# Kernel optimization log

Measured on AMD Instinct MI355X. Metric: run time of the kernel, lower is better.

## Reference

```python
import jax, jax.numpy as jnp
import numpy as np

B, N, T, NUM_API = 4, 160, 512, 20000  # queries, list length, tag vocab size, number of APIs
TAG_DENSITY = 0.05


def _compute_lambda(y_score, tag_set, M):
    # y_score: [N]; tag_set: [N,T] multi-hot rows api_tag_embedding[y_pred]; M: [T] multi-hot target.
    # Faithful to mode == 'cover' branch of LambdaRankLoss.compute_lambda.
    n = tag_set.shape[0]
    f32 = tag_set.dtype
    idx = jnp.arange(n)
    log_values = jnp.log2(jnp.arange(2, n + 2, dtype=f32))             # [N]
    P = jax.lax.cummax(tag_set, axis=0)                                # set_union_list = cummax(tag_set) [N,T]
    Mc = (jnp.count_nonzero(M) + 1).astype(f32)                        # M_nonzero_count
    # count_nonzero(clamp(M - set_union_list[k], min=0)) == #(M_t > P[k,t])
    cU = jnp.sum(M[None, :] > P, axis=1).astype(f32)                   # [N]

    # pre[i] = rowwise-max of tag_set[:i-1]. Torch quirk: i==0 -> tag_set[:-1] (all but last row); i==1 -> empty.
    pre = jnp.where(idx[:, None] == 0, P[n - 2][None, :],
                    jnp.where(idx[:, None] == 1, jnp.zeros((), f32),
                              P[jnp.clip(idx - 2, 0, n - 1)]))         # [N,T] (0 is max-identity: entries >= 0)

    # R[a,b] = max(tag_set[a..b]) along rows; 0 when b < a (rows before a masked to 0, then cummax)
    masked = jnp.where(idx[None, :, None] >= idx[:, None, None], tag_set[None, :, :], jnp.zeros((), f32))
    R = jax.lax.cummax(masked, axis=1)                                 # [N,N,T]

    # mid[k,i] = max(tag_set[i+1:k]) = R[i+1, k-1] when k >= i+2, else empty -> 0
    i_ix = idx[None, :]
    k_ix = idx[:, None]
    mid = jnp.where((k_ix >= i_ix + 2)[:, :, None],
                    R[jnp.clip(i_ix + 1, 0, n - 1), jnp.clip(k_ix - 1, 0, n - 1)],
                    jnp.zeros((), f32))                                # [K,I,T]

    # A[k,i] = max(cat(tag_set[:i-1], tag_set[i+1:k]));  Q[k,i,j] = max(A[k,i], tag_set[j])
    A = jnp.maximum(pre[None, :, :], mid)                              # [K,I,T]
    # count_nonzero(clamp(M - Q[k,i,j], 0)) = sum_t [M_t > A[k,i,t]] * [M_t > tag_set[j,t]]
    aM = (M[None, None, :] > A).astype(f32)                            # [K,I,T]
    bM = (M[None, :] > tag_set).astype(f32)                            # [J,T]
    cQ = jnp.einsum('kit,jt->kij', aM, bM)                             # [K,I,J] Q_nonzero counts

    W = (cU[:, None, None] - cQ) / (Mc * log_values[:, None, None])    # [K,I,J]
    # Z1[i,j] = sum_{k=i}^{j-1} W[k,i,j]  (strictly upper-triangular in (i,j))
    maskZ = (idx[None, :, None] <= idx[:, None, None]) & (idx[:, None, None] < idx[None, None, :])
    Z1 = jnp.sum(jnp.where(maskZ, W, jnp.zeros((), f32)), axis=0)      # [I,J]

    # lambda1[i,j] = 1 / (1 + exp(s_i - s_j))
    lam = 1.0 / (1.0 + jnp.exp(y_score[:, None] - y_score[None, :]))
    return jnp.sum(lam * Z1) / jnp.asarray(n + 1, f32)


def setup_inputs() -> dict:
    key = jax.random.key(0)
    k1, k2, k3, k4 = jax.random.split(key, 4)
    y_scores = jax.random.normal(k1, (B, N), jnp.float32)
    y_preds = jax.random.randint(k2, (B, N), 0, NUM_API)
    M = (jax.random.uniform(k3, (B, T)) < TAG_DENSITY).astype(jnp.float32)
    api_tag_embedding = (jax.random.uniform(k4, (NUM_API, T)) < TAG_DENSITY).astype(jnp.float32)
    return {"y_scores": y_scores, "M": M, "api_tag_embedding": api_tag_embedding, "y_preds": y_preds}


def reference(y_scores, M, api_tag_embedding, y_preds):
    def per_query(s, m, pred):
        return _compute_lambda(s, api_tag_embedding[pred], m)
    vals = jax.vmap(per_query)(y_scores, M, y_preds)  # [B]
    return jnp.mean(vals)  # loss / len(y_scores)
```

## Files before the change

### kernel.cpp

```cpp
#include <hip/hip_runtime.h>
#include <stdint.h>

typedef unsigned long long u64;

constexpr int B_ = 4;
constexpr int N_ = 160;
constexpr int T_ = 512;
constexpr int W_ = T_ / 64;

__global__ __launch_bounds__(64) void pack_tags(const float* __restrict__ emb,
                                                const int* __restrict__ preds,
                                                u64* __restrict__ tags) {
    int row  = blockIdx.x;
    int lane = threadIdx.x;
    const float* src = emb + (long long)preds[row] * T_;
#pragma unroll
    for (int w = 0; w < W_; ++w) {
        float v = src[w * 64 + lane];
        u64 m = __ballot(v != 0.0f);
        if (lane == 0) tags[(long long)row * W_ + w] = m;
    }
}

__global__ __launch_bounds__(256) void pack_scan(const float* __restrict__ Mf,
                                                 const u64* __restrict__ tags,
                                                 u64* __restrict__ Mp,
                                                 u64* __restrict__ P,
                                                 float* __restrict__ cU,
                                                 float* __restrict__ Mc) {
    __shared__ u64 S0[N_ * W_];
    __shared__ u64 S1[N_ * W_];
    __shared__ u64 Msh[W_];

    const int b    = blockIdx.x;
    const int tid  = threadIdx.x;
    const int lane = tid & 63;
    const int wv   = tid >> 6;

    for (int w = wv; w < W_; w += 4) {
        float v = Mf[(long long)b * T_ + w * 64 + lane];
        u64 m = __ballot(v != 0.0f);
        if (lane == 0) { Msh[w] = m; Mp[b * W_ + w] = m; }
    }
    for (int x = tid; x < N_ * W_; x += 256)
        S0[x] = tags[(long long)b * N_ * W_ + x];
    __syncthreads();

    u64* src = S0;
    u64* dst = S1;
    for (int d = 1; d < N_; d <<= 1) {
        for (int x = tid; x < N_ * W_; x += 256) {
            int r = x >> 3;
            u64 v = src[x];
            if (r >= d) v |= src[x - d * W_];
            dst[x] = v;
        }
        __syncthreads();
        u64* t = src; src = dst; dst = t;
    }

    for (int x = tid; x < N_ * W_; x += 256)
        P[(long long)b * N_ * W_ + x] = src[x];

    if (tid < N_) {
        int c = 0;
#pragma unroll
        for (int w = 0; w < W_; ++w)
            c += __popcll(Msh[w] & ~src[tid * W_ + w]);
        cU[b * N_ + tid] = (float)c;
    }
    if (tid == 0) {
        int c = 0;
#pragma unroll
        for (int w = 0; w < W_; ++w) c += __popcll(Msh[w]);
        Mc[b] = (float)(c + 1);
    }
}

__global__ __launch_bounds__(256) void lambda_main(const u64* __restrict__ tags,
                                                   const u64* __restrict__ Mp,
                                                   const u64* __restrict__ P,
                                                   const float* __restrict__ cU,
                                                   const float* __restrict__ Mc,
                                                   const float* __restrict__ scores,
                                                   double* __restrict__ partials) {
    constexpr int LD = N_ + 1;
    __shared__ u64 tagsT[W_ * LD];
    __shared__ u64 bufA[W_ * LD];
    __shared__ u64 bufB[W_ * LD];
    __shared__ u64 awT[W_ * LD];
    __shared__ u64 bT[W_ * LD];
    __shared__ u64 Msh[W_];
    __shared__ float scoresL[N_];
    __shared__ float redF[4];

    const int k   = blockIdx.x;
    const int b   = blockIdx.y;
    const int tid = threadIdx.x;

    if (tid < W_)  Msh[tid]    = Mp[b * W_ + tid];
    if (tid < N_)  scoresL[tid] = scores[b * N_ + tid];

    for (int x = tid; x < W_ * N_; x += 256) {
        int r = x >> 3, w = x & 7;
        tagsT[w * LD + r] = tags[(long long)b * N_ * W_ + x];
    }
    __syncthreads();

    for (int x = tid; x < W_ * N_; x += 256) {
        int r = x >> 3, w = x & 7;
        bufA[w * LD + r] = (r < k) ? tagsT[w * LD + r] : 0ull;
    }
    __syncthreads();

    u64* src = bufA;
    u64* dst = bufB;
    for (int d = 1; d < N_; d <<= 1) {
        for (int x = tid; x < W_ * N_; x += 256) {
            int r = x >> 3, w = x & 7;
            u64 v = src[w * LD + r];
            if (r + d < k) v |= src[w * LD + r + d];
            dst[w * LD + r] = v;
        }
        __syncthreads();
        u64* t = src; src = dst; dst = t;
    }

    for (int x = tid; x < W_ * N_; x += 256) {
        int i = x >> 3, w = x & 7;
        u64 pre;
        if (i == 1) pre = 0ull;
        else {
            int sr = (i == 0) ? (N_ - 2) : (i - 2);
            pre = P[((long long)b * N_ + sr) * W_ + w];
        }
        u64 sv = (i + 1 < k) ? src[w * LD + i + 1] : 0ull;
        awT[w * LD + i] = Msh[w] & ~pre & ~sv;
        bT[w * LD + i]  = Msh[w] & ~tagsT[w * LD + i];
    }
    __syncthreads();

    const int m = N_ - 1 - k;
    float accLam = 0.0f, accC = 0.0f;
    if (m > 0) {
        const int npairs = (k + 1) * m;
        if (tid < npairs) {
            int cnt = (npairs - tid + 255) >> 8;
            int i   = tid / m;
            int jj  = tid - i * m;
            const int di = 256 / m;
            const int rj = 256 - di * m;
            for (int c = 0; c < cnt; ++c) {
                const int j = k + 1 + jj;
                int cc = 0;
#pragma unroll
                for (int w = 0; w < W_; ++w)
                    cc += __popcll(awT[w * LD + i] & bT[w * LD + j]);
                float lam = 1.0f / (1.0f + __expf(scoresL[i] - scoresL[j]));
                accLam += lam;
                accC   += lam * (float)cc;
                i += di; jj += rj;
                if (jj >= m) { jj -= m; ++i; }
            }
        }
    }

    const float cUk = cU[b * N_ + k];
    float val = cUk * accLam - accC;
    for (int off = 32; off >= 1; off >>= 1) val += __shfl_down(val, off, 64);
    if ((tid & 63) == 0) redF[tid >> 6] = val;
    __syncthreads();
    if (tid == 0) {
        float s = redF[0] + redF[1] + redF[2] + redF[3];
        float invlog = 1.0f / log2f((float)(k + 2));
        partials[b * N_ + k] = (double)(s * invlog) / (double)Mc[b];
    }
}

__global__ __launch_bounds__(256) void finalize(const double* __restrict__ partials,
                                                float* __restrict__ out) {
    __shared__ double redD[4];
    const int tid = threadIdx.x;
    double s = 0.0;
    for (int x = tid; x < B_ * N_; x += 256) s += partials[x];
    for (int off = 32; off >= 1; off >>= 1) s += __shfl_down(s, off, 64);
    if ((tid & 63) == 0) redD[tid >> 6] = s;
    __syncthreads();
    if (tid == 0) {
        double t = redD[0] + redD[1] + redD[2] + redD[3];
        out[0] = (float)(t / ((double)(N_ + 1) * (double)B_));
    }
}

extern "C" void kernel_launch(void* const* d_in, const int* in_sizes, int n_in,
                              void* d_out, int out_size, void* d_ws, size_t ws_size,
                              hipStream_t stream) {
    const float* y_scores = (const float*)d_in[0];
    const float* Mf       = (const float*)d_in[1];
    const float* emb      = (const float*)d_in[2];
    const int*   preds    = (const int*)d_in[3];
    float* out = (float*)d_out;

    u64* tags = (u64*)d_ws;
    u64* P    = tags + (size_t)B_ * N_ * W_;
    u64* Mp   = P + (size_t)B_ * N_ * W_;
    double* partials = (double*)(Mp + B_ * W_);
    float* cU = (float*)(partials + B_ * N_);
    float* Mc = cU + B_ * N_;

    pack_tags<<<B_ * N_, 64, 0, stream>>>(emb, preds, tags);
    pack_scan<<<B_, 256, 0, stream>>>(Mf, tags, Mp, P, cU, Mc);
    dim3 grid(N_, B_);
    lambda_main<<<grid, 256, 0, stream>>>(tags, Mp, P, cU, Mc, y_scores, partials);
    finalize<<<1, 256, 0, stream>>>(partials, out);
}
```

Baseline: 113.6 us.

## Fuse pipeline into two kernels with in-block prefix scan and atomic final reduction

```diff
diff --git a/kernel.cpp b/kernel.cpp
--- a/kernel.cpp
+++ b/kernel.cpp
@@ -8,135 +8,118 @@
 constexpr int T_ = 512;
 constexpr int W_ = T_ / 64;
 
-__global__ __launch_bounds__(64) void pack_tags(const float* __restrict__ emb,
-                                                const int* __restrict__ preds,
-                                                u64* __restrict__ tags) {
+__global__ __launch_bounds__(64) void pack_all(const float* __restrict__ emb,
+                                               const int* __restrict__ preds,
+                                               const float* __restrict__ Mf,
+                                               u64* __restrict__ tags,
+                                               u64* __restrict__ Mp,
+                                               double* __restrict__ accD,
+                                               int* __restrict__ cnt) {
     int row  = blockIdx.x;
     int lane = threadIdx.x;
-    const float* src = emb + (long long)preds[row] * T_;
+    if (row < B_ * N_) {
+        const float* src = emb + (long long)preds[row] * T_;
 #pragma unroll
-    for (int w = 0; w < W_; ++w) {
-        float v = src[w * 64 + lane];
-        u64 m = __ballot(v != 0.0f);
-        if (lane == 0) tags[(long long)row * W_ + w] = m;
-    }
-}
-
-__global__ __launch_bounds__(256) void pack_scan(const float* __restrict__ Mf,
-                                                 const u64* __restrict__ tags,
-                                                 u64* __restrict__ Mp,
-                                                 u64* __restrict__ P,
-                                                 float* __restrict__ cU,
-                                                 float* __restrict__ Mc) {
-    __shared__ u64 S0[N_ * W_];
-    __shared__ u64 S1[N_ * W_];
-    __shared__ u64 Msh[W_];
-
-    const int b    = blockIdx.x;
-    const int tid  = threadIdx.x;
-    const int lane = tid & 63;
-    const int wv   = tid >> 6;
-
-    for (int w = wv; w < W_; w += 4) {
-        float v = Mf[(long long)b * T_ + w * 64 + lane];
-        u64 m = __ballot(v != 0.0f);
-        if (lane == 0) { Msh[w] = m; Mp[b * W_ + w] = m; }
-    }
-    for (int x = tid; x < N_ * W_; x += 256)
-        S0[x] = tags[(long long)b * N_ * W_ + x];
-    __syncthreads();
-
-    u64* src = S0;
-    u64* dst = S1;
-    for (int d = 1; d < N_; d <<= 1) {
-        for (int x = tid; x < N_ * W_; x += 256) {
-            int r = x >> 3;
-            u64 v = src[x];
-            if (r >= d) v |= src[x - d * W_];
-            dst[x] = v;
+        for (int w = 0; w < W_; ++w) {
+            u64 m = __ballot(src[w * 64 + lane] != 0.0f);
+            if (lane == 0) tags[(long long)row * W_ + w] = m;
         }
-        __syncthreads();
-        u64* t = src; src = dst; dst = t;
-    }
-
-    for (int x = tid; x < N_ * W_; x += 256)
-        P[(long long)b * N_ * W_ + x] = src[x];
-
-    if (tid < N_) {
-        int c = 0;
+    } else {
+        int b = row - B_ * N_;
+        const float* src = Mf + (long long)b * T_;
 #pragma unroll
-        for (int w = 0; w < W_; ++w)
-            c += __popcll(Msh[w] & ~src[tid * W_ + w]);
-        cU[b * N_ + tid] = (float)c;
-    }
-    if (tid == 0) {
-        int c = 0;
-#pragma unroll
-        for (int w = 0; w < W_; ++w) c += __popcll(Msh[w]);
-        Mc[b] = (float)(c + 1);
+        for (int w = 0; w < W_; ++w) {
+            u64 m = __ballot(src[w * 64 + lane] != 0.0f);
+            if (lane == 0) Mp[b * W_ + w] = m;
+        }
+        if (b == 0 && lane == 0) { accD[0] = 0.0; cnt[0] = 0; }
     }
 }
 
 __global__ __launch_bounds__(256) void lambda_main(const u64* __restrict__ tags,
                                                    const u64* __restrict__ Mp,
-                                                   const u64* __restrict__ P,
-                                                   const float* __restrict__ cU,
-                                                   const float* __restrict__ Mc,
                                                    const float* __restrict__ scores,
-                                                   double* __restrict__ partials) {
+                                                   double* __restrict__ accD,
+                                                   int* __restrict__ cnt,
+                                                   float* __restrict__ out) {
     constexpr int LD = N_ + 1;
-    __shared__ u64 tagsT[W_ * LD];
-    __shared__ u64 bufA[W_ * LD];
-    __shared__ u64 bufB[W_ * LD];
-    __shared__ u64 awT[W_ * LD];
+    __shared__ u64 Tsh[W_ * LD];
+    __shared__ u64 U[W_ * LD];
+    __shared__ u64 V[W_ * LD];
     __shared__ u64 bT[W_ * LD];
     __shared__ u64 Msh[W_];
     __shared__ float scoresL[N_];
     __shared__ float redF[4];
+    __shared__ float cUsh, Mcsh;
 
     const int k   = blockIdx.x;
     const int b   = blockIdx.y;
     const int tid = threadIdx.x;
 
-    if (tid < W_)  Msh[tid]    = Mp[b * W_ + tid];
+    if (tid < W_)  Msh[tid]     = Mp[b * W_ + tid];
     if (tid < N_)  scoresL[tid] = scores[b * N_ + tid];
 
     for (int x = tid; x < W_ * N_; x += 256) {
         int r = x >> 3, w = x & 7;
-        tagsT[w * LD + r] = tags[(long long)b * N_ * W_ + x];
+        Tsh[w * LD + r] = tags[(long long)b * N_ * W_ + x];
     }
     __syncthreads();
 
     for (int x = tid; x < W_ * N_; x += 256) {
         int r = x >> 3, w = x & 7;
-        bufA[w * LD + r] = (r < k) ? tagsT[w * LD + r] : 0ull;
+        bT[w * LD + r] = Msh[w] & ~Tsh[w * LD + r];
     }
-    __syncthreads();
 
-    u64* src = bufA;
-    u64* dst = bufB;
+    u64* rd = Tsh;
+    u64* wr = U;
+    for (int d = 1; d < k; d <<= 1) {
+        for (int x = tid; x < W_ * k; x += 256) {
+            int r = x >> 3, w = x & 7;
+            u64 v = rd[w * LD + r];
+            if (r + d < k) v |= rd[w * LD + r + d];
+            wr[w * LD + r] = v;
+        }
+        __syncthreads();
+        rd = wr;
+        wr = (rd == U) ? V : U;
+    }
+    u64* suf = rd;
+    u64* freebuf = wr;
+
+    u64* prd = Tsh;
+    u64* pwr = freebuf;
     for (int d = 1; d < N_; d <<= 1) {
         for (int x = tid; x < W_ * N_; x += 256) {
             int r = x >> 3, w = x & 7;
-            u64 v = src[w * LD + r];
-            if (r + d < k) v |= src[w * LD + r + d];
-            dst[w * LD + r] = v;
+            u64 v = prd[w * LD + r];
+            if (r >= d) v |= prd[w * LD + r - d];
+            pwr[w * LD + r] = v;
         }
         __syncthreads();
-        u64* t = src; src = dst; dst = t;
+        u64* t = prd; prd = pwr; pwr = t;
     }
 
-    for (int x = tid; x < W_ * N_; x += 256) {
+    u64* aw = pwr;
+    for (int x = tid; x < W_ * (k + 1); x += 256) {
         int i = x >> 3, w = x & 7;
         u64 pre;
         if (i == 1) pre = 0ull;
         else {
             int sr = (i == 0) ? (N_ - 2) : (i - 2);
-            pre = P[((long long)b * N_ + sr) * W_ + w];
+            pre = prd[w * LD + sr];
         }
-        u64 sv = (i + 1 < k) ? src[w * LD + i + 1] : 0ull;
-        awT[w * LD + i] = Msh[w] & ~pre & ~sv;
-        bT[w * LD + i]  = Msh[w] & ~tagsT[w * LD + i];
+        u64 sv = (i + 1 < k) ? suf[w * LD + i + 1] : 0ull;
+        aw[w * LD + i] = Msh[w] & ~pre & ~sv;
+    }
+    if (tid == 0) {
+        int c = 0, cm = 0;
+#pragma unroll
+        for (int w = 0; w < W_; ++w) {
+            c  += __popcll(Msh[w] & ~prd[w * LD + k]);
+            cm += __popcll(Msh[w]);
+        }
+        cUsh = (float)c;
+        Mcsh = (float)(cm + 1);
     }
     __syncthreads();
 
@@ -145,17 +128,17 @@
     if (m > 0) {
         const int npairs = (k + 1) * m;
         if (tid < npairs) {
-            int cnt = (npairs - tid + 255) >> 8;
+            int cntp = (npairs - tid + 255) >> 8;
             int i   = tid / m;
             int jj  = tid - i * m;
             const int di = 256 / m;
             const int rj = 256 - di * m;
-            for (int c = 0; c < cnt; ++c) {
+            for (int c = 0; c < cntp; ++c) {
                 const int j = k + 1 + jj;
                 int cc = 0;
 #pragma unroll
                 for (int w = 0; w < W_; ++w)
-                    cc += __popcll(awT[w * LD + i] & bT[w * LD + j]);
+                    cc += __popcll(aw[w * LD + i] & bT[w * LD + j]);
                 float lam = 1.0f / (1.0f + __expf(scoresL[i] - scoresL[j]));
                 accLam += lam;
                 accC   += lam * (float)cc;
@@ -165,30 +148,21 @@
         }
     }
 
-    const float cUk = cU[b * N_ + k];
-    float val = cUk * accLam - accC;
+    float val = cUsh * accLam - accC;
     for (int off = 32; off >= 1; off >>= 1) val += __shfl_down(val, off, 64);
     if ((tid & 63) == 0) redF[tid >> 6] = val;
     __syncthreads();
     if (tid == 0) {
         float s = redF[0] + redF[1] + redF[2] + redF[3];
         float invlog = 1.0f / log2f((float)(k + 2));
-        partials[b * N_ + k] = (double)(s * invlog) / (double)Mc[b];
-    }
-}
-
-__global__ __launch_bounds__(256) void finalize(const double* __restrict__ partials,
-                                                float* __restrict__ out) {
-    __shared__ double redD[4];
-    const int tid = threadIdx.x;
-    double s = 0.0;
-    for (int x = tid; x < B_ * N_; x += 256) s += partials[x];
-    for (int off = 32; off >= 1; off >>= 1) s += __shfl_down(s, off, 64);
-    if ((tid & 63) == 0) redD[tid >> 6] = s;
-    __syncthreads();
-    if (tid == 0) {
-        double t = redD[0] + redD[1] + redD[2] + redD[3];
-        out[0] = (float)(t / ((double)(N_ + 1) * (double)B_));
+        double v = (double)(s * invlog) / (double)Mcsh;
+        atomicAdd(accD, v);
+        __threadfence();
+        int c = atomicAdd(cnt, 1);
+        if (c == B_ * N_ - 1) {
+            double total = atomicAdd(accD, 0.0);
+            out[0] = (float)(total / ((double)(N_ + 1) * (double)B_));
+        }
     }
 }
 
@@ -201,16 +175,12 @@
     const int*   preds    = (const int*)d_in[3];
     float* out = (float*)d_out;
 
-    u64* tags = (u64*)d_ws;
-    u64* P    = tags + (size_t)B_ * N_ * W_;
-    u64* Mp   = P + (size_t)B_ * N_ * W_;
-    double* partials = (double*)(Mp + B_ * W_);
-    float* cU = (float*)(partials + B_ * N_);
-    float* Mc = cU + B_ * N_;
+    u64* tags   = (u64*)d_ws;
+    u64* Mp     = tags + (size_t)B_ * N_ * W_;
+    double* accD = (double*)(Mp + B_ * W_);
+    int* cnt    = (int*)(accD + 1);
 
-    pack_tags<<<B_ * N_, 64, 0, stream>>>(emb, preds, tags);
-    pack_scan<<<B_, 256, 0, stream>>>(Mf, tags, Mp, P, cU, Mc);
+    pack_all<<<B_ * N_ + B_, 64, 0, stream>>>(emb, preds, Mf, tags, Mp, accD, cnt);
     dim3 grid(N_, B_);
-    lambda_main<<<grid, 256, 0, stream>>>(tags, Mp, P, cU, Mc, y_scores, partials);
-    finalize<<<1, 256, 0, stream>>>(partials, out);
+    lambda_main<<<grid, 256, 0, stream>>>(tags, Mp, y_scores, accD, cnt, out);
 }
```

Measured after the change: 111.3 us. 2.0% less time.
